# Optimization experiments

Hardware: AMD Instinct MI355X
Metric: run time of the kernel (lower is better)

The kernel has to match this reference:

```python
import jax, jax.numpy as jnp
import numpy as np

B, N, KNN_K = 4, 4096, 32
C1, C = 128, 256
K_SLOTS, RECON_M, N_RECON = 4, 96, 128
SLOT_ITERS = 3

def _ln(x, g, b):
    m = x.mean(-1, keepdims=True)
    v = jnp.var(x, axis=-1, keepdims=True)
    return (x - m) * jax.lax.rsqrt(v + 1e-5) * g + b

def _gather(f, idx):
    # f [B,P,C], idx [B,N,K] -> [B,N,K,C]
    return jax.vmap(lambda a, i: a[i])(f, idx)

def _knn(xyz, k):
    sq = jnp.sum(xyz * xyz, -1)
    d = sq[:, :, None] + sq[:, None, :] - 2.0 * jnp.einsum('bnc,bmc->bnm', xyz, xyz)
    return jax.lax.top_k(-d, k)[1]

def _conv_block(xyz, feats, W, b):
    # InterZPConv-style: KNN neighbor gather -> per-neighbor transform -> max aggregate
    idx = _knn(xyz, KNN_K)
    rel = _gather(xyz, idx) - xyz[:, :, None, :]
    h = jnp.concatenate([_gather(feats, idx), rel], axis=-1)
    h = jax.nn.relu(jnp.einsum('bnkc,cd->bnkd', h, W) + b)
    return h.max(axis=2)

def _bn(x, g, b):
    # BatchNorm2d (training mode) over (batch, slot) axes for 1x1-conv stacks
    m = x.mean(axis=(0, 1), keepdims=True)
    v = jnp.var(x, axis=(0, 1), keepdims=True)
    return (x - m) * jax.lax.rsqrt(v + 1e-5) * g + b

def _gru(upd, prev, W_ih, W_hh, b_ih, b_hh):
    gi = upd @ W_ih + b_ih
    gh = prev @ W_hh + b_hh
    r = jax.nn.sigmoid(gi[..., :C] + gh[..., :C])
    z = jax.nn.sigmoid(gi[..., C:2 * C] + gh[..., C:2 * C])
    n = jnp.tanh(gi[..., 2 * C:] + r * gh[..., 2 * C:])
    return (1.0 - z) * n + z * prev

def _chamfer(a, b):
    # a [B,M,3], b [B,P,3] -> (min over b per a-point, min over a per b-point), squared dists
    d = jnp.sum((a[..., :, None, :] - b[..., None, :, :]) ** 2, axis=-1)
    return d.min(axis=-1), d.min(axis=-2)

def _fps(pts):
    # farthest point sampling of N_RECON points from pts [P,3]
    P = pts.shape[0]
    d0 = jnp.full((P,), 1e10, pts.dtype)
    def step(carry, _):
        d, last = carry
        d = jnp.minimum(d, jnp.sum((pts - pts[last]) ** 2, axis=-1))
        nxt = jnp.argmax(d).astype(jnp.int32)
        return (d, nxt), nxt
    _, idxs = jax.lax.scan(step, (d0, jnp.array(0, jnp.int32)), None, length=N_RECON - 1)
    return jnp.concatenate([jnp.zeros((1,), jnp.int32), idxs])

def setup_inputs() -> dict:
    key = jax.random.key(0)
    ks = jax.random.split(key, 16)
    w = lambda k, s: jax.random.normal(k, s, jnp.float32) * 0.02
    z = lambda *s: jnp.zeros(s, jnp.float32)
    o = lambda *s: jnp.ones(s, jnp.float32)
    return {
        'x': jax.random.normal(ks[0], (B, 3, N), jnp.float32),
        'pose': jnp.zeros((B, N, 4, 4), jnp.float32),
        'W1': w(ks[1], (1 + 3, C1)), 'b1': z(C1),
        'W2': w(ks[2], (C1 + 3, C)), 'b2': z(C),
        'slots_mu': w(ks[3], (1, 1, C)), 'slots_sigma': jnp.abs(w(ks[4], (1, 1, C))) + 0.01,
        'ln_in_g': o(C), 'ln_in_b': z(C),
        'ln_slot_g': o(C), 'ln_slot_b': z(C),
        'ln_ff_g': o(C), 'ln_ff_b': z(C),
        'Wq': w(ks[5], (C, C)), 'Wk': w(ks[6], (C, C)), 'Wv': w(ks[7], (C, C)),
        'W_ih': w(ks[8], (C, 3 * C)), 'W_hh': w(ks[9], (C, 3 * C)),
        'b_ih': z(3 * C), 'b_hh': z(3 * C),
        'Wm1': w(ks[10], (C, C)), 'bm1': z(C),
        'Wm2': w(ks[11], (C, C)), 'bm2': z(C),
        'Wr1': w(ks[12], (C, C)), 'br1': z(C), 'g1': o(C), 'be1': z(C),
        'Wr2': w(ks[13], (C, C)), 'br2': z(C), 'g2': o(C), 'be2': z(C),
        'Wr3': w(ks[14], (C, RECON_M * 3)), 'br3': z(RECON_M * 3),
    }

def reference(x, pose, W1, b1, W2, b2, slots_mu, slots_sigma, ln_in_g, ln_in_b,
              ln_slot_g, ln_slot_b, ln_ff_g, ln_ff_b, Wq, Wk, Wv,
              W_ih, W_hh, b_ih, b_hh, Wm1, bm1, Wm2, bm2,
              Wr1, br1, g1, be1, Wr2, br2, g2, be2, Wr3, br3):
    xyz = jnp.transpose(x, (0, 2, 1))  # [B,N,3]
    feats = jnp.ones((B, N, 1), x.dtype)  # preprocess_input: unit features, na=1
    f = _conv_block(xyz, feats, W1, b1)   # [B,N,C1]
    f = _conv_block(xyz, f, W2, b2)       # [B,N,C]
    # Slot attention over per-point invariant features
    inp = _ln(f, ln_in_g, ln_in_b)
    kk = inp @ Wk
    vv = inp @ Wv
    slots = slots_mu + slots_sigma * jax.random.normal(jax.random.key(42), (B, K_SLOTS, C), x.dtype)
    scale = C ** -0.5
    attn = None
    for _ in range(SLOT_ITERS):
        prev = slots
        q = _ln(slots, ln_slot_g, ln_slot_b) @ Wq
        logits = scale * jnp.einsum('bkc,bnc->bkn', q, kk)
        attn = jax.nn.softmax(logits, axis=1)  # softmax over slots
        wgt = attn / (attn.sum(axis=-1, keepdims=True) + 1e-8)
        upd = jnp.einsum('bkn,bnc->bkc', wgt, vv)
        slots = _gru(upd, prev, W_ih, W_hh, b_ih, b_hh)
        h = _ln(slots, ln_ff_g, ln_ff_b)
        slots = slots + (jax.nn.relu(h @ Wm1 + bm1) @ Wm2 + bm2)
    attn_out = jnp.transpose(attn, (0, 2, 1))  # [B,N,K] (attn_ori.transpose(1,2))
    # Part reconstruction net (1x1 conv + BN + ReLU stack on slot features)
    h = jax.nn.relu(_bn(slots @ Wr1 + br1, g1, be1))
    h = jax.nn.relu(_bn(h @ Wr2 + br2, g2, be2))
    slot_points = (h @ Wr3 + br3).reshape(B, K_SLOTS, RECON_M, 3)
    all_pts = slot_points.reshape(B, K_SLOTS * RECON_M, 3)
    # FPS downsample + global chamfer against input points
    idx = jax.vmap(_fps)(all_pts)  # [B, N_RECON]
    ds = jnp.take_along_axis(all_pts, idx[..., None], axis=1)  # [B,N_RECON,3]
    d1, d2 = _chamfer(ds, xyz)
    loss = (d1.mean(-1) + d2.mean(-1)).mean()
    return loss, attn_out
```

## Files before the change

### kernel.cpp

```cpp
#include <hip/hip_runtime.h>

#define NBATCH 4
#define NPTS   4096
#define KNNK   32
#define C1D    128
#define CD     256
#define KPAD   160
#define ASTR   168
#define ASTR2  264

typedef _Float16 v8h __attribute__((ext_vector_type(8)));
typedef float    v4f __attribute__((ext_vector_type(4)));
typedef unsigned long long ull;


__device__ __forceinline__ float block_sum256(float v, float* red) {
    #pragma unroll
    for (int o = 32; o; o >>= 1) v += __shfl_down(v, o);
    __syncthreads();
    if ((threadIdx.x & 63) == 0) red[threadIdx.x >> 6] = v;
    __syncthreads();
    return red[0] + red[1] + red[2] + red[3];
}

__device__ __forceinline__ unsigned rotl32(unsigned x, unsigned r) {
    return (x << r) | (x >> (32u - r));
}

__device__ float erfinv_f(float x) {
    float w = -log1pf(-x * x);
    float p;
    if (w < 5.0f) {
        w -= 2.5f;
        p = 2.81022636e-08f;
        p = fmaf(p, w, 3.43273939e-07f);
        p = fmaf(p, w, -3.5233877e-06f);
        p = fmaf(p, w, -4.39150654e-06f);
        p = fmaf(p, w, 0.00021858087f);
        p = fmaf(p, w, -0.00125372503f);
        p = fmaf(p, w, -0.00417768164f);
        p = fmaf(p, w, 0.246640727f);
        p = fmaf(p, w, 1.50140941f);
    } else {
        w = sqrtf(w) - 3.0f;
        p = -0.000200214257f;
        p = fmaf(p, w, 0.000100950558f);
        p = fmaf(p, w, 0.00134934322f);
        p = fmaf(p, w, -0.00367342844f);
        p = fmaf(p, w, 0.00573950773f);
        p = fmaf(p, w, -0.0076224613f);
        p = fmaf(p, w, 0.00943887047f);
        p = fmaf(p, w, 1.00167406f);
        p = fmaf(p, w, 2.83297682f);
    }
    return p * x;
}

__device__ __forceinline__ float bits_to_normal(unsigned bits) {
    unsigned fb = (bits >> 9) | 0x3f800000u;
    float f = __uint_as_float(fb) - 1.0f;
    const float lo = -0.99999994f;
    float u = fmaf(f, 2.0f, lo);
    u = fmaxf(u, lo);
    return 1.41421356237f * erfinv_f(u);
}

__device__ __forceinline__ unsigned fmap(float f) {
    unsigned b = __float_as_uint(f);
    return (b & 0x80000000u) ? ~b : (b | 0x80000000u);
}

template <int CTRL, int RM>
__device__ __forceinline__ ull dpp_min_u64(ull k) {
    unsigned lo = (unsigned)k, hi = (unsigned)(k >> 32);
    unsigned tlo = (unsigned)__builtin_amdgcn_update_dpp((int)lo, (int)lo, CTRL, RM, 0xf, false);
    unsigned thi = (unsigned)__builtin_amdgcn_update_dpp((int)hi, (int)hi, CTRL, RM, 0xf, false);
    ull t = ((ull)thi << 32) | tlo;
    return t < k ? t : k;
}

template <int CTRL, int RM>
__device__ __forceinline__ void dpp_lexmax(float& v, int& ix) {
    int tv = __builtin_amdgcn_update_dpp(__float_as_int(v), __float_as_int(v), CTRL, RM, 0xf, false);
    int ti = __builtin_amdgcn_update_dpp(ix, ix, CTRL, RM, 0xf, false);
    float fv = __int_as_float(tv);
    bool take = (fv > v) || (fv == v && ti < ix);
    v  = take ? fv : v;
    ix = take ? ti : ix;
}


__global__ void prep_kernel(const float* __restrict__ x, float* __restrict__ xyz,
                            float4* __restrict__ xyzw) {
    int gid = blockIdx.x * 256 + threadIdx.x;
    if (gid >= NBATCH * NPTS) return;
    int b = gid >> 12, n = gid & (NPTS - 1);
    float a0 = x[(b * 3 + 0) * NPTS + n];
    float a1 = x[(b * 3 + 1) * NPTS + n];
    float a2 = x[(b * 3 + 2) * NPTS + n];
    xyz[gid * 3 + 0] = a0; xyz[gid * 3 + 1] = a1; xyz[gid * 3 + 2] = a2;
    float sq = a0 * a0 + a1 * a1 + a2 * a2;
    xyzw[gid] = make_float4(a0, a1, a2, sq);
}

__global__ void slots_init_kernel(const float* __restrict__ mu, const float* __restrict__ sg,
                                  float* __restrict__ slots, float* __restrict__ asum) {
    int j = blockIdx.x * 256 + threadIdx.x;
    if (j < 16) asum[j] = 0.0f;
    if (j >= 2048) return;
    unsigned ks0 = 0u, ks1 = 42u, ks2 = 0u ^ 42u ^ 0x1BD11BDAu;
    unsigned x0 = (unsigned)j + ks0;
    unsigned x1 = (unsigned)(j + 2048) + ks1;
    #define RND(r) { x0 += x1; x1 = rotl32(x1, r); x1 ^= x0; }
    RND(13u) RND(15u) RND(26u) RND(6u);  x0 += ks1; x1 += ks2 + 1u;
    RND(17u) RND(29u) RND(16u) RND(24u); x0 += ks2; x1 += ks0 + 2u;
    RND(13u) RND(15u) RND(26u) RND(6u);  x0 += ks0; x1 += ks1 + 3u;
    RND(17u) RND(29u) RND(16u) RND(24u); x0 += ks1; x1 += ks2 + 4u;
    RND(13u) RND(15u) RND(26u) RND(6u);  x0 += ks2; x1 += ks0 + 5u;
    #undef RND
    int c0 = j & 255, c1 = (j + 2048) & 255;
    slots[j]        = mu[c0] + sg[c0] * bits_to_normal(x0);
    slots[j + 2048] = mu[c1] + sg[c1] * bits_to_normal(x1);
}

__global__ __launch_bounds__(256) void knn_kernel(const float4* __restrict__ xyzw,
                                                  int* __restrict__ knn_idx) {
    int wid = threadIdx.x >> 6, lane = threadIdx.x & 63;
    int pid = blockIdx.x * 4 + wid;
    int b = pid >> 12, n = pid & (NPTS - 1);
    const float4* xb = xyzw + (size_t)b * NPTS;
    float4 p = xb[n];
    unsigned d[64];
    #pragma unroll
    for (int i = 0; i < 64; ++i) {
        float4 c = xb[i * 64 + lane];
        float dot = p.x * c.x + p.y * c.y + p.z * c.z;
        d[i] = fmap(p.w + c.w - 2.0f * dot);
    }
    unsigned gv[8]; int gi[8];
    #pragma unroll
    for (int g = 0; g < 8; ++g) {
        unsigned mv = d[g * 8]; int mi = g * 8;
        #pragma unroll
        for (int j = 1; j < 8; ++j)
            if (d[g * 8 + j] < mv) { mv = d[g * 8 + j]; mi = g * 8 + j; }
        gv[g] = mv; gi[g] = mi * 64 + lane;
    }
    unsigned lv = gv[0]; int li = gi[0];
    #pragma unroll
    for (int g = 1; g < 8; ++g)
        if (gv[g] < lv) { lv = gv[g]; li = gi[g]; }

    int* out = knn_idx + (size_t)pid * KNNK;
    #pragma unroll 1
    for (int s = 0; s < KNNK; ++s) {
        ull k = ((ull)lv << 32) | (unsigned)li;
        k = dpp_min_u64<0x111, 0xf>(k);
        k = dpp_min_u64<0x112, 0xf>(k);
        k = dpp_min_u64<0x114, 0xf>(k);
        k = dpp_min_u64<0x118, 0xf>(k);
        k = dpp_min_u64<0x142, 0xa>(k);
        k = dpp_min_u64<0x143, 0xc>(k);
        int fm = __builtin_amdgcn_readlane((int)(unsigned)k, 63);
        if (lane == 0) out[s] = fm;
        int flane = fm & 63;
        int slot  = fm >> 6;
        if (lane == flane) {
            int g = slot >> 3;
            #pragma unroll
            for (int g2 = 0; g2 < 8; ++g2) {
                if (g2 == g) {
                    #pragma unroll
                    for (int j = 0; j < 8; ++j)
                        if (g2 * 8 + j == slot) d[g2 * 8 + j] = 0xFFFFFFFFu;
                    unsigned mv = d[g2 * 8]; int mi = g2 * 8;
                    #pragma unroll
                    for (int j = 1; j < 8; ++j)
                        if (d[g2 * 8 + j] < mv) { mv = d[g2 * 8 + j]; mi = g2 * 8 + j; }
                    gv[g2] = mv; gi[g2] = mi * 64 + lane;
                }
            }
            lv = gv[0]; li = gi[0];
            #pragma unroll
            for (int g2 = 1; g2 < 8; ++g2)
                if (gv[g2] < lv) { lv = gv[g2]; li = gi[g2]; }
        }
    }
}

__global__ __launch_bounds__(128) void conv1_kernel(const float* __restrict__ xyz,
                                                    const int* __restrict__ knn_idx,
                                                    const float* __restrict__ W1,
                                                    const float* __restrict__ b1,
                                                    _Float16* __restrict__ f1h) {
    int pid = blockIdx.x;
    int b = pid >> 12, n = pid & (NPTS - 1);
    int d = threadIdx.x, lane = threadIdx.x & 63;
    const float* xb = xyz + (size_t)b * NPTS * 3;
    float w0 = W1[d], wx = W1[C1D + d], wy = W1[2 * C1D + d], wz = W1[3 * C1D + d];
    float bb = b1[d];
    float px = xb[n * 3], py = xb[n * 3 + 1], pz = xb[n * 3 + 2];
    const int* idx = knn_idx + (size_t)pid * KNNK;
    float cx = 0.0f, cy = 0.0f, cz = 0.0f;
    if (lane < 32) {
        int j = idx[lane];
        cx = xb[j * 3]; cy = xb[j * 3 + 1]; cz = xb[j * 3 + 2];
    }
    float m = -1e30f;
    #pragma unroll
    for (int k = 0; k < KNNK; ++k) {
        float jx = __shfl(cx, k), jy = __shfl(cy, k), jz = __shfl(cz, k);
        float v = w0 + bb + (jx - px) * wx + (jy - py) * wy + (jz - pz) * wz;
        m = fmaxf(m, v);
    }
    f1h[(size_t)pid * C1D + d] = (_Float16)fmaxf(m, 0.0f);
}

__global__ void w2t_kernel(const float* __restrict__ W2, _Float16* __restrict__ W2t) {
    int n = blockIdx.x;
    int k = threadIdx.x;
    W2t[n * KPAD + k] = (k < 131) ? (_Float16)W2[k * CD + n] : (_Float16)0.0f;
}

__global__ void wkvt_kernel(const float* __restrict__ Wk, const float* __restrict__ Wv,
                            _Float16* __restrict__ WkvT) {
    int n = blockIdx.x;
    int c = threadIdx.x;
    float v = (n < 256) ? Wk[c * CD + n] : Wv[c * CD + (n - 256)];
    WkvT[n * CD + c] = (_Float16)v;
}

__global__ __launch_bounds__(256) void conv2_mfma_kernel(const float* __restrict__ xyz,
                                                         const _Float16* __restrict__ f1h,
                                                         const int* __restrict__ knn_idx,
                                                         const _Float16* __restrict__ W2t,
                                                         const float* __restrict__ b2,
                                                         const float* __restrict__ g_in,
                                                         const float* __restrict__ b_in,
                                                         _Float16* __restrict__ inph) {
    __shared__ _Float16 A[64 * ASTR];
    __shared__ float colmax[2 * CD];
    __shared__ float red[4];
    int pid2 = blockIdx.x;
    int gp0 = pid2 * 2;
    int b = gp0 >> 12, n0 = gp0 & (NPTS - 1);
    int tid = threadIdx.x;
    const int* idx = knn_idx + (size_t)pid2 * 64;
    const float* xb = xyz + (size_t)b * NPTS * 3;

    {
        int r = tid & 63, seg = tid >> 6;
        int j = idx[r];
        const uint4* s4 = (const uint4*)(f1h + ((size_t)b * NPTS + j) * C1D);
        uint4* d4 = (uint4*)&A[r * ASTR];
        #pragma unroll
        for (int i = 0; i < 4; ++i) d4[seg * 4 + i] = s4[seg * 4 + i];
        unsigned* z = (unsigned*)&A[r * ASTR + 128];
        for (int i = seg; i < 20; i += 4) z[i] = 0u;
        int np_ = (r < 32) ? n0 : (n0 + 1);
        if (seg == 0) {
            A[r * ASTR + 128] = (_Float16)(xb[j * 3 + 0] - xb[np_ * 3 + 0]);
            A[r * ASTR + 129] = (_Float16)(xb[j * 3 + 1] - xb[np_ * 3 + 1]);
        } else if (seg == 1) {
            A[r * ASTR + 130] = (_Float16)(xb[j * 3 + 2] - xb[np_ * 3 + 2]);
        }
    }
    __syncthreads();

    int w = tid >> 6, lane = tid & 63, quad = lane >> 4, lr = lane & 15;
    v4f acc[4][4];
    #pragma unroll
    for (int rt = 0; rt < 4; ++rt)
        #pragma unroll
        for (int ct = 0; ct < 4; ++ct)
            acc[rt][ct] = (v4f){0.0f, 0.0f, 0.0f, 0.0f};

    #pragma unroll
    for (int kk = 0; kk < KPAD; kk += 32) {
        v8h af[4], bf[4];
        #pragma unroll
        for (int rt = 0; rt < 4; ++rt)
            af[rt] = *(const v8h*)&A[(rt * 16 + lr) * ASTR + kk + quad * 8];
        #pragma unroll
        for (int ct = 0; ct < 4; ++ct) {
            int ncol = w * 64 + ct * 16 + lr;
            bf[ct] = *(const v8h*)(W2t + (size_t)ncol * KPAD + kk + quad * 8);
        }
        #pragma unroll
        for (int rt = 0; rt < 4; ++rt)
            #pragma unroll
            for (int ct = 0; ct < 4; ++ct)
                acc[rt][ct] = __builtin_amdgcn_mfma_f32_16x16x32_f16(af[rt], bf[ct], acc[rt][ct], 0, 0, 0);
    }

    #pragma unroll
    for (int ct = 0; ct < 4; ++ct) {
        float tm[4];
        #pragma unroll
        for (int rt = 0; rt < 4; ++rt) {
            v4f a = acc[rt][ct];
            float v = fmaxf(fmaxf(a[0], a[1]), fmaxf(a[2], a[3]));
            v = fmaxf(v, __shfl_xor(v, 16));
            v = fmaxf(v, __shfl_xor(v, 32));
            tm[rt] = v;
        }
        float p0 = fmaxf(tm[0], tm[1]);
        float p1 = fmaxf(tm[2], tm[3]);
        if (quad == 0) {
            colmax[0 * CD + w * 64 + ct * 16 + lr] = p0;
            colmax[1 * CD + w * 64 + ct * 16 + lr] = p1;
        }
    }
    __syncthreads();

    int d = tid;
    #pragma unroll
    for (int p = 0; p < 2; ++p) {
        float v = fmaxf(colmax[p * CD + d] + b2[d], 0.0f);
        float s = block_sum256(v, red);
        float mean = s * (1.0f / 256.0f);
        float s2 = block_sum256(v * v, red);
        float var = s2 * (1.0f / 256.0f) - mean * mean;
        float iv = (v - mean) * rsqrtf(var + 1e-5f) * g_in[d] + b_in[d];
        inph[(size_t)(gp0 + p) * CD + d] = (_Float16)iv;
    }
}

__global__ __launch_bounds__(256) void kv_mfma_kernel(const _Float16* __restrict__ inph,
                                                      const _Float16* __restrict__ WkvT,
                                                      float* __restrict__ kk,
                                                      float* __restrict__ vv) {
    __shared__ _Float16 A[64 * ASTR2];
    int rb = blockIdx.x >> 1, half = blockIdx.x & 1;
    int row0 = rb * 64;
    int tid = threadIdx.x;
    {
        const uint4* src4 = (const uint4*)(inph + (size_t)row0 * CD);
        #pragma unroll
        for (int i = 0; i < 8; ++i) {
            int idx = i * 256 + tid;
            int row = idx >> 5, c8 = idx & 31;
            *(uint4*)&A[row * ASTR2 + c8 * 8] = src4[idx];
        }
    }
    __syncthreads();
    int w = tid >> 6, lane = tid & 63, quad = lane >> 4, lr = lane & 15;
    v4f acc[4][4];
    #pragma unroll
    for (int rt = 0; rt < 4; ++rt)
        #pragma unroll
        for (int ct = 0; ct < 4; ++ct)
            acc[rt][ct] = (v4f){0.0f, 0.0f, 0.0f, 0.0f};
    #pragma unroll
    for (int ks = 0; ks < CD; ks += 32) {
        v8h af[4], bf[4];
        #pragma unroll
        for (int rt = 0; rt < 4; ++rt)
            af[rt] = *(const v8h*)&A[(rt * 16 + lr) * ASTR2 + ks + quad * 8];
        #pragma unroll
        for (int ct = 0; ct < 4; ++ct) {
            int ncol = half * 256 + w * 64 + ct * 16 + lr;
            bf[ct] = *(const v8h*)(WkvT + (size_t)ncol * CD + ks + quad * 8);
        }
        #pragma unroll
        for (int rt = 0; rt < 4; ++rt)
            #pragma unroll
            for (int ct = 0; ct < 4; ++ct)
                acc[rt][ct] = __builtin_amdgcn_mfma_f32_16x16x32_f16(af[rt], bf[ct], acc[rt][ct], 0, 0, 0);
    }
    float* dst = half ? vv : kk;
    #pragma unroll
    for (int rt = 0; rt < 4; ++rt)
        #pragma unroll
        for (int ct = 0; ct < 4; ++ct) {
            int col = w * 64 + ct * 16 + lr;
            #pragma unroll
            for (int r = 0; r < 4; ++r) {
                int row = rt * 16 + quad * 4 + r;
                dst[(size_t)(row0 + row) * CD + col] = acc[rt][ct][r];
            }
        }
}

__global__ __launch_bounds__(256) void slotq_kernel(const float* __restrict__ slots,
                                                    const float* __restrict__ g_sl,
                                                    const float* __restrict__ b_sl,
                                                    const float* __restrict__ Wq,
                                                    float* __restrict__ q) {
    int row = blockIdx.x;
    int d = threadIdx.x;
    __shared__ float sl[CD];
    __shared__ float red[4];
    float v = slots[row * CD + d];
    float s = block_sum256(v, red);
    float mean = s * (1.0f / 256.0f);
    float s2 = block_sum256(v * v, red);
    float var = s2 * (1.0f / 256.0f) - mean * mean;
    float ln = (v - mean) * rsqrtf(var + 1e-5f) * g_sl[d] + b_sl[d];
    sl[d] = ln;
    __syncthreads();
    float acc = 0.0f;
    const float4* sp = (const float4*)sl;
    for (int c4 = 0; c4 < 64; ++c4) {
        float4 x = sp[c4];
        int cb = c4 * 4;
        acc += x.x * Wq[cb * CD + d] + x.y * Wq[(cb + 1) * CD + d]
             + x.z * Wq[(cb + 2) * CD + d] + x.w * Wq[(cb + 3) * CD + d];
    }
    q[row * CD + d] = acc;
}

__global__ __launch_bounds__(256) void attn_updp_kernel(const float* __restrict__ q,
                                                        const float* __restrict__ kk,
                                                        const float* __restrict__ vv,
                                                        float* __restrict__ asum,
                                                        float* __restrict__ updp,
                                                        float* __restrict__ out_attn) {
    int b = blockIdx.x >> 4;
    int chunk = blockIdx.x & 15;
    int t = threadIdx.x;
    __shared__ float qs[4 * CD];
    __shared__ float aw[256 * 4];
    __shared__ float redk[16];
    for (int i = t; i < 4 * CD; i += 256) qs[i] = q[b * 4 * CD + i];
    __syncthreads();

    int n = chunk * 256 + t;
    const float4* kp = (const float4*)(kk + ((size_t)b * NPTS + n) * CD);
    const float4* q0 = (const float4*)(qs);
    const float4* q1 = (const float4*)(qs + CD);
    const float4* q2 = (const float4*)(qs + 2 * CD);
    const float4* q3 = (const float4*)(qs + 3 * CD);
    float a0 = 0, a1 = 0, a2 = 0, a3 = 0;
    for (int c4 = 0; c4 < 64; ++c4) {
        float4 kv = kp[c4];
        float4 x;
        x = q0[c4]; a0 += kv.x * x.x + kv.y * x.y + kv.z * x.z + kv.w * x.w;
        x = q1[c4]; a1 += kv.x * x.x + kv.y * x.y + kv.z * x.z + kv.w * x.w;
        x = q2[c4]; a2 += kv.x * x.x + kv.y * x.y + kv.z * x.z + kv.w * x.w;
        x = q3[c4]; a3 += kv.x * x.x + kv.y * x.y + kv.z * x.z + kv.w * x.w;
    }
    const float scale = 0.0625f;
    float l0 = scale * a0, l1 = scale * a1, l2 = scale * a2, l3 = scale * a3;
    float mx = fmaxf(fmaxf(l0, l1), fmaxf(l2, l3));
    float e0 = expf(l0 - mx), e1 = expf(l1 - mx), e2 = expf(l2 - mx), e3 = expf(l3 - mx);
    float inv = 1.0f / (e0 + e1 + e2 + e3);
    e0 *= inv; e1 *= inv; e2 *= inv; e3 *= inv;
    aw[t * 4 + 0] = e0; aw[t * 4 + 1] = e1; aw[t * 4 + 2] = e2; aw[t * 4 + 3] = e3;
    if (out_attn) {
        float* o = out_attn + ((size_t)b * NPTS + n) * 4;
        o[0] = e0; o[1] = e1; o[2] = e2; o[3] = e3;
    }
    float as[4] = {e0, e1, e2, e3};
    #pragma unroll
    for (int k = 0; k < 4; ++k) {
        float v = as[k];
        #pragma unroll
        for (int o = 32; o; o >>= 1) v += __shfl_down(v, o);
        if ((t & 63) == 0) redk[(t >> 6) * 4 + k] = v;
    }
    __syncthreads();
    if (t < 4) {
        float s = redk[t] + redk[4 + t] + redk[8 + t] + redk[12 + t];
        atomicAdd(&asum[b * 4 + t], s);
    }

    float ac0 = 0.0f, ac1 = 0.0f, ac2 = 0.0f, ac3 = 0.0f;
    const float* vb = vv + ((size_t)b * NPTS + chunk * 256) * CD;
    for (int nn2 = 0; nn2 < 256; ++nn2) {
        float v = vb[(size_t)nn2 * CD + t];
        float4 w4 = *(const float4*)&aw[nn2 * 4];
        ac0 += w4.x * v; ac1 += w4.y * v; ac2 += w4.z * v; ac3 += w4.w * v;
    }
    updp[((size_t)(b * 4 + 0) * 16 + chunk) * CD + t] = ac0;
    updp[((size_t)(b * 4 + 1) * 16 + chunk) * CD + t] = ac1;
    updp[((size_t)(b * 4 + 2) * 16 + chunk) * CD + t] = ac2;
    updp[((size_t)(b * 4 + 3) * 16 + chunk) * CD + t] = ac3;
}

__global__ __launch_bounds__(256) void gru_gates_kernel(const float* __restrict__ updp,
                                                        const float* __restrict__ asum,
                                                        const float* __restrict__ slots,
                                                        const float* __restrict__ W_ih,
                                                        const float* __restrict__ W_hh,
                                                        const float* __restrict__ b_ih,
                                                        const float* __restrict__ b_hh,
                                                        float* __restrict__ gi,
                                                        float* __restrict__ gh) {
    int row = blockIdx.x / 3, gate = blockIdx.x % 3;
    int d = threadIdx.x;
    __shared__ float su[CD], sp[CD];
    float f = 1.0f / (asum[row] + 1e-8f);
    float u = 0.0f;
    for (int p = 0; p < 16; ++p) u += updp[((size_t)row * 16 + p) * CD + d];
    u *= f;
    su[d] = u; sp[d] = slots[row * CD + d];
    __syncthreads();
    float acc_i = b_ih[gate * CD + d];
    float acc_h = b_hh[gate * CD + d];
    const float* wi = W_ih + gate * CD + d;
    const float* wh = W_hh + gate * CD + d;
    for (int c = 0; c < CD; ++c) {
        acc_i += su[c] * wi[c * 3 * CD];
        acc_h += sp[c] * wh[c * 3 * CD];
    }
    gi[row * 3 * CD + gate * CD + d] = acc_i;
    gh[row * 3 * CD + gate * CD + d] = acc_h;
}

__global__ __launch_bounds__(256) void gru_mlp_kernel(const float* __restrict__ gi,
                                                      const float* __restrict__ gh,
                                                      float* __restrict__ slots,
                                                      const float* __restrict__ g_ff,
                                                      const float* __restrict__ b_ff,
                                                      const float* __restrict__ Wm1,
                                                      const float* __restrict__ bm1,
                                                      const float* __restrict__ Wm2,
                                                      const float* __restrict__ bm2,
                                                      float* __restrict__ asum) {
    int row = blockIdx.x;
    int d = threadIdx.x;
    __shared__ float sh[CD];
    __shared__ float red[4];
    float prev = slots[row * CD + d];
    float gir = gi[row * 3 * CD + d], giz = gi[row * 3 * CD + CD + d], gin = gi[row * 3 * CD + 2 * CD + d];
    float ghr = gh[row * 3 * CD + d], ghz = gh[row * 3 * CD + CD + d], ghn = gh[row * 3 * CD + 2 * CD + d];
    if (d == 0) asum[row] = 0.0f;
    float r = 1.0f / (1.0f + expf(-(gir + ghr)));
    float z = 1.0f / (1.0f + expf(-(giz + ghz)));
    float nn = tanhf(gin + r * ghn);
    float sNew = (1.0f - z) * nn + z * prev;
    float s = block_sum256(sNew, red);
    float mean = s * (1.0f / 256.0f);
    float s2 = block_sum256(sNew * sNew, red);
    float var = s2 * (1.0f / 256.0f) - mean * mean;
    float h = (sNew - mean) * rsqrtf(var + 1e-5f) * g_ff[d] + b_ff[d];
    __syncthreads();
    sh[d] = h;
    __syncthreads();
    float y = bm1[d];
    {
        const float4* hp = (const float4*)sh;
        for (int c4 = 0; c4 < 64; ++c4) {
            float4 x = hp[c4];
            int cb = c4 * 4;
            y += x.x * Wm1[cb * CD + d] + x.y * Wm1[(cb + 1) * CD + d]
               + x.z * Wm1[(cb + 2) * CD + d] + x.w * Wm1[(cb + 3) * CD + d];
        }
    }
    y = fmaxf(y, 0.0f);
    __syncthreads();
    sh[d] = y;
    __syncthreads();
    float o = bm2[d];
    {
        const float4* hp = (const float4*)sh;
        for (int c4 = 0; c4 < 64; ++c4) {
            float4 x = hp[c4];
            int cb = c4 * 4;
            o += x.x * Wm2[cb * CD + d] + x.y * Wm2[(cb + 1) * CD + d]
               + x.z * Wm2[(cb + 2) * CD + d] + x.w * Wm2[(cb + 3) * CD + d];
        }
    }
    slots[row * CD + d] = sNew + o;
}

__global__ __launch_bounds__(320) void recon_kernel(const float* __restrict__ slots,
                                                    const float* __restrict__ Wr1, const float* __restrict__ br1,
                                                    const float* __restrict__ g1, const float* __restrict__ be1,
                                                    const float* __restrict__ Wr2, const float* __restrict__ br2,
                                                    const float* __restrict__ g2, const float* __restrict__ be2,
                                                    const float* __restrict__ Wr3, const float* __restrict__ br3,
                                                    float* __restrict__ spts) {
    __shared__ float sl[16 * CD];
    __shared__ float h1[16 * CD];
    __shared__ float h2[16 * CD];
    int d = threadIdx.x;
    if (d < CD) for (int r = 0; r < 16; ++r) sl[r * CD + d] = slots[r * CD + d];
    __syncthreads();
    if (d < CD) {
        float t[16];
        #pragma unroll
        for (int r = 0; r < 16; ++r) t[r] = br1[d];
        for (int c4 = 0; c4 < 64; ++c4) {
            int cb = c4 * 4;
            float w0 = Wr1[cb * CD + d], w1 = Wr1[(cb + 1) * CD + d];
            float w2 = Wr1[(cb + 2) * CD + d], w3 = Wr1[(cb + 3) * CD + d];
            #pragma unroll
            for (int r = 0; r < 16; ++r) {
                float4 x = *(const float4*)(sl + r * CD + cb);
                t[r] += x.x * w0 + x.y * w1 + x.z * w2 + x.w * w3;
            }
        }
        float mean = 0.0f;
        for (int r = 0; r < 16; ++r) mean += t[r];
        mean *= (1.0f / 16.0f);
        float var = 0.0f;
        for (int r = 0; r < 16; ++r) { float dd = t[r] - mean; var += dd * dd; }
        var *= (1.0f / 16.0f);
        float inv = rsqrtf(var + 1e-5f);
        for (int r = 0; r < 16; ++r)
            h1[r * CD + d] = fmaxf(0.0f, (t[r] - mean) * inv * g1[d] + be1[d]);
    }
    __syncthreads();
    if (d < CD) {
        float t[16];
        #pragma unroll
        for (int r = 0; r < 16; ++r) t[r] = br2[d];
        for (int c4 = 0; c4 < 64; ++c4) {
            int cb = c4 * 4;
            float w0 = Wr2[cb * CD + d], w1 = Wr2[(cb + 1) * CD + d];
            float w2 = Wr2[(cb + 2) * CD + d], w3 = Wr2[(cb + 3) * CD + d];
            #pragma unroll
            for (int r = 0; r < 16; ++r) {
                float4 x = *(const float4*)(h1 + r * CD + cb);
                t[r] += x.x * w0 + x.y * w1 + x.z * w2 + x.w * w3;
            }
        }
        float mean = 0.0f;
        for (int r = 0; r < 16; ++r) mean += t[r];
        mean *= (1.0f / 16.0f);
        float var = 0.0f;
        for (int r = 0; r < 16; ++r) { float dd = t[r] - mean; var += dd * dd; }
        var *= (1.0f / 16.0f);
        float inv = rsqrtf(var + 1e-5f);
        for (int r = 0; r < 16; ++r)
            h2[r * CD + d] = fmaxf(0.0f, (t[r] - mean) * inv * g2[d] + be2[d]);
    }
    __syncthreads();
    if (d < 288) {
        float t[16];
        #pragma unroll
        for (int r = 0; r < 16; ++r) t[r] = br3[d];
        for (int c4 = 0; c4 < 64; ++c4) {
            int cb = c4 * 4;
            float w0 = Wr3[cb * 288 + d], w1 = Wr3[(cb + 1) * 288 + d];
            float w2 = Wr3[(cb + 2) * 288 + d], w3 = Wr3[(cb + 3) * 288 + d];
            #pragma unroll
            for (int r = 0; r < 16; ++r) {
                float4 x = *(const float4*)(h2 + r * CD + cb);
                t[r] += x.x * w0 + x.y * w1 + x.z * w2 + x.w * w3;
            }
        }
        for (int r = 0; r < 16; ++r) spts[r * 288 + d] = t[r];
    }
}

__global__ __launch_bounds__(64) void fps_kernel(const float* __restrict__ spts,
                                                 int* __restrict__ fidx,
                                                 float* __restrict__ lacc,
                                                 unsigned* __restrict__ mnbuf) {
    int b = blockIdx.x;
    int lane = threadIdx.x;
    const float* pts = spts + (size_t)b * 384 * 3;
    int* out = fidx + b * 128;
    if (lane == 0) out[0] = 0;
    if (b == 0 && lane == 0) lacc[0] = 0.0f;
    mnbuf[b * 128 + lane] = 0x7F800000u;
    mnbuf[b * 128 + 64 + lane] = 0x7F800000u;
    float px[6], py[6], pz[6], dd[6];
    #pragma unroll
    for (int i = 0; i < 6; ++i) {
        int m = i * 64 + lane;
        px[i] = pts[m * 3]; py[i] = pts[m * 3 + 1]; pz[i] = pts[m * 3 + 2];
        dd[i] = 1e10f;
    }
    float lx = pts[0], ly = pts[1], lz = pts[2];
    #pragma unroll 1
    for (int s = 1; s < 128; ++s) {
        #pragma unroll
        for (int i = 0; i < 6; ++i) {
            float dx = px[i] - lx, dy = py[i] - ly, dz = pz[i] - lz;
            dd[i] = fminf(dd[i], dx * dx + dy * dy + dz * dz);
        }
        float bv = dd[0]; int bi = lane;
        #pragma unroll
        for (int i = 1; i < 6; ++i)
            if (dd[i] > bv) { bv = dd[i]; bi = i * 64 + lane; }
        dpp_lexmax<0x111, 0xf>(bv, bi);
        dpp_lexmax<0x112, 0xf>(bv, bi);
        dpp_lexmax<0x114, 0xf>(bv, bi);
        dpp_lexmax<0x118, 0xf>(bv, bi);
        dpp_lexmax<0x142, 0xa>(bv, bi);
        dpp_lexmax<0x143, 0xc>(bv, bi);
        int fm = __builtin_amdgcn_readlane(bi, 63);
        if (lane == 0) out[s] = fm;
        int slot = fm >> 6, sl_lane = fm & 63;
        float sx = px[0], sy = py[0], sz = pz[0];
        #pragma unroll
        for (int i = 1; i < 6; ++i)
            if (slot == i) { sx = px[i]; sy = py[i]; sz = pz[i]; }
        lx = __int_as_float(__builtin_amdgcn_readlane(__float_as_int(sx), sl_lane));
        ly = __int_as_float(__builtin_amdgcn_readlane(__float_as_int(sy), sl_lane));
        lz = __int_as_float(__builtin_amdgcn_readlane(__float_as_int(sz), sl_lane));
    }
}

__global__ __launch_bounds__(256) void chamfer_sum2_kernel(const float* __restrict__ spts,
                                                           const int* __restrict__ fidx,
                                                           const float* __restrict__ xyz,
                                                           float* __restrict__ lacc) {
    int b = blockIdx.x >> 4, chunk = blockIdx.x & 15;
    int t = threadIdx.x;
    __shared__ float ds[128 * 3];
    __shared__ float red[4];
    const float* pts = spts + (size_t)b * 384 * 3;
    if (t < 128) {
        int j = fidx[b * 128 + t];
        ds[t * 3] = pts[j * 3]; ds[t * 3 + 1] = pts[j * 3 + 1]; ds[t * 3 + 2] = pts[j * 3 + 2];
    }
    __syncthreads();
    int n = chunk * 256 + t;
    const float* xb = xyz + (size_t)b * NPTS * 3;
    float px = xb[n * 3], py = xb[n * 3 + 1], pz = xb[n * 3 + 2];
    float mn = 1e30f;
    #pragma unroll 4
    for (int jj = 0; jj < 128; ++jj) {
        float dx = ds[jj * 3] - px, dy = ds[jj * 3 + 1] - py, dz = ds[jj * 3 + 2] - pz;
        mn = fminf(mn, dx * dx + dy * dy + dz * dz);
    }
    float total = block_sum256(mn * (1.0f / 4096.0f), red);
    if (t == 0) atomicAdd(lacc, total);
}

__global__ __launch_bounds__(128) void chamfer_min1_kernel(const float* __restrict__ spts,
                                                           const int* __restrict__ fidx,
                                                           const float* __restrict__ xyz,
                                                           unsigned* __restrict__ mnbuf) {
    int b = blockIdx.x >> 4, chunk = blockIdx.x & 15;
    int t = threadIdx.x;
    __shared__ float tile[256 * 3];
    const float* xb = xyz + ((size_t)b * NPTS + chunk * 256) * 3;
    for (int i = t; i < 768; i += 128) tile[i] = xb[i];
    __syncthreads();
    int j = fidx[b * 128 + t];
    const float* pts = spts + (size_t)b * 384 * 3;
    float px = pts[j * 3], py = pts[j * 3 + 1], pz = pts[j * 3 + 2];
    float mn = 1e30f;
    #pragma unroll 4
    for (int i = 0; i < 256; ++i) {
        float dx = tile[i * 3] - px, dy = tile[i * 3 + 1] - py, dz = tile[i * 3 + 2] - pz;
        mn = fminf(mn, dx * dx + dy * dy + dz * dz);
    }
    atomicMin(&mnbuf[b * 128 + t], __float_as_uint(mn));
}

__global__ __launch_bounds__(512) void chamfer_final_kernel(const unsigned* __restrict__ mnbuf,
                                                            const float* __restrict__ lacc,
                                                            float* __restrict__ out) {
    int t = threadIdx.x;
    __shared__ float r[8];
    float v = __uint_as_float(mnbuf[t]) * (1.0f / 128.0f);
    #pragma unroll
    for (int o = 32; o; o >>= 1) v += __shfl_down(v, o);
    if ((t & 63) == 0) r[t >> 6] = v;
    __syncthreads();
    if (t == 0) {
        float tot = 0.0f;
        #pragma unroll
        for (int i = 0; i < 8; ++i) tot += r[i];
        out[0] = (lacc[0] + tot) * 0.25f;
    }
}


extern "C" void kernel_launch(void* const* d_in, const int* in_sizes, int n_in,
                              void* d_out, int out_size, void* d_ws, size_t ws_size,
                              hipStream_t stream) {
    (void)in_sizes; (void)n_in; (void)out_size; (void)ws_size;
    const float* x    = (const float*)d_in[0];
    const float* W1   = (const float*)d_in[2];
    const float* b1   = (const float*)d_in[3];
    const float* W2   = (const float*)d_in[4];
    const float* b2   = (const float*)d_in[5];
    const float* mu   = (const float*)d_in[6];
    const float* sg   = (const float*)d_in[7];
    const float* g_in = (const float*)d_in[8];
    const float* b_in = (const float*)d_in[9];
    const float* g_sl = (const float*)d_in[10];
    const float* b_sl = (const float*)d_in[11];
    const float* g_ff = (const float*)d_in[12];
    const float* b_ff = (const float*)d_in[13];
    const float* Wq   = (const float*)d_in[14];
    const float* Wk   = (const float*)d_in[15];
    const float* Wv   = (const float*)d_in[16];
    const float* W_ih = (const float*)d_in[17];
    const float* W_hh = (const float*)d_in[18];
    const float* b_ih = (const float*)d_in[19];
    const float* b_hh = (const float*)d_in[20];
    const float* Wm1  = (const float*)d_in[21];
    const float* bm1  = (const float*)d_in[22];
    const float* Wm2  = (const float*)d_in[23];
    const float* bm2  = (const float*)d_in[24];
    const float* Wr1  = (const float*)d_in[25];
    const float* br1  = (const float*)d_in[26];
    const float* g1   = (const float*)d_in[27];
    const float* be1  = (const float*)d_in[28];
    const float* Wr2  = (const float*)d_in[29];
    const float* br2  = (const float*)d_in[30];
    const float* g2   = (const float*)d_in[31];
    const float* be2  = (const float*)d_in[32];
    const float* Wr3  = (const float*)d_in[33];
    const float* br3  = (const float*)d_in[34];

    float* ws    = (float*)d_ws;
    float* xyz   = ws;
    float* xyzw  = xyz + 49152;
    int*   knn   = (int*)(xyzw + 65536);
    _Float16* f1h = (_Float16*)(knn + 524288);
    _Float16* W2t = (_Float16*)((float*)f1h + 1048576);
    _Float16* WkvT = (_Float16*)((float*)W2t + 20480);
    _Float16* inph = (_Float16*)((float*)WkvT + 65536);
    float* kkb   = (float*)inph + 2097152;
    float* vvb   = kkb + 4194304;
    float* slots = vvb + 4194304;
    float* qb    = slots + 4096;
    float* asum  = qb + 4096;
    float* updp  = asum + 16;
    float* gi    = updp + 65536;
    float* gh    = gi + 12288;
    float* spts  = gh + 12288;
    int*   fidx  = (int*)(spts + 4608);
    float* lacc  = (float*)(fidx + 512);
    unsigned* mnbuf = (unsigned*)(lacc + 1);

    float* out = (float*)d_out;

    prep_kernel<<<64, 256, 0, stream>>>(x, xyz, (float4*)xyzw);
    slots_init_kernel<<<8, 256, 0, stream>>>(mu, sg, slots, asum);
    knn_kernel<<<NBATCH * NPTS / 4, 256, 0, stream>>>((const float4*)xyzw, knn);
    conv1_kernel<<<NBATCH * NPTS, 128, 0, stream>>>(xyz, knn, W1, b1, f1h);
    w2t_kernel<<<256, 160, 0, stream>>>(W2, W2t);
    wkvt_kernel<<<512, 256, 0, stream>>>(Wk, Wv, WkvT);
    conv2_mfma_kernel<<<NBATCH * NPTS / 2, 256, 0, stream>>>(xyz, f1h, knn, W2t, b2, g_in, b_in, inph);
    kv_mfma_kernel<<<NBATCH * NPTS / 64 * 2, 256, 0, stream>>>(inph, WkvT, kkb, vvb);

    for (int it = 0; it < 3; ++it) {
        slotq_kernel<<<16, 256, 0, stream>>>(slots, g_sl, b_sl, Wq, qb);
        attn_updp_kernel<<<64, 256, 0, stream>>>(qb, kkb, vvb, asum, updp,
                                                 (it == 2) ? (out + 1) : (float*)nullptr);
        gru_gates_kernel<<<48, 256, 0, stream>>>(updp, asum, slots, W_ih, W_hh, b_ih, b_hh, gi, gh);
        gru_mlp_kernel<<<16, 256, 0, stream>>>(gi, gh, slots, g_ff, b_ff, Wm1, bm1, Wm2, bm2, asum);
    }

    recon_kernel<<<1, 320, 0, stream>>>(slots, Wr1, br1, g1, be1, Wr2, br2, g2, be2, Wr3, br3, spts);
    fps_kernel<<<4, 64, 0, stream>>>(spts, fidx, lacc, mnbuf);
    chamfer_sum2_kernel<<<64, 256, 0, stream>>>(spts, fidx, xyz, lacc);
    chamfer_min1_kernel<<<64, 128, 0, stream>>>(spts, fidx, xyz, mnbuf);
    chamfer_final_kernel<<<1, 512, 0, stream>>>(mnbuf, lacc, out);
}
```

Measured before the change: 741.6 us.

## Merge small kernels and spread slot-attention and GRU gate work over more blocks

Folds slot initialisation into prep_kernel, merges the two weight-transpose kernels into one, and merges the two chamfer kernels into one launch, removing several launches. The attention kernel now uses 256 blocks with one wave per slot and 64 points per block instead of 64 blocks, and the GRU gate kernel splits its reduction into halves over 96 blocks. Both are meant to raise parallelism in the latency-bound slot iterations. In exchange, the partial-sum buffers grow and the GRU gate kernel has to sum 64 partials instead of 16.

```diff
diff --git a/kernel.cpp b/kernel.cpp
--- a/kernel.cpp
+++ b/kernel.cpp
@@ -91,7 +91,9 @@
 
 
 __global__ void prep_kernel(const float* __restrict__ x, float* __restrict__ xyz,
-                            float4* __restrict__ xyzw) {
+                            float4* __restrict__ xyzw,
+                            const float* __restrict__ mu, const float* __restrict__ sg,
+                            float* __restrict__ slots, float* __restrict__ asum) {
     int gid = blockIdx.x * 256 + threadIdx.x;
     if (gid >= NBATCH * NPTS) return;
     int b = gid >> 12, n = gid & (NPTS - 1);
@@ -101,26 +103,23 @@
     xyz[gid * 3 + 0] = a0; xyz[gid * 3 + 1] = a1; xyz[gid * 3 + 2] = a2;
     float sq = a0 * a0 + a1 * a1 + a2 * a2;
     xyzw[gid] = make_float4(a0, a1, a2, sq);
-}
-
-__global__ void slots_init_kernel(const float* __restrict__ mu, const float* __restrict__ sg,
-                                  float* __restrict__ slots, float* __restrict__ asum) {
-    int j = blockIdx.x * 256 + threadIdx.x;
-    if (j < 16) asum[j] = 0.0f;
-    if (j >= 2048) return;
-    unsigned ks0 = 0u, ks1 = 42u, ks2 = 0u ^ 42u ^ 0x1BD11BDAu;
-    unsigned x0 = (unsigned)j + ks0;
-    unsigned x1 = (unsigned)(j + 2048) + ks1;
-    #define RND(r) { x0 += x1; x1 = rotl32(x1, r); x1 ^= x0; }
-    RND(13u) RND(15u) RND(26u) RND(6u);  x0 += ks1; x1 += ks2 + 1u;
-    RND(17u) RND(29u) RND(16u) RND(24u); x0 += ks2; x1 += ks0 + 2u;
-    RND(13u) RND(15u) RND(26u) RND(6u);  x0 += ks0; x1 += ks1 + 3u;
-    RND(17u) RND(29u) RND(16u) RND(24u); x0 += ks1; x1 += ks2 + 4u;
-    RND(13u) RND(15u) RND(26u) RND(6u);  x0 += ks2; x1 += ks0 + 5u;
-    #undef RND
-    int c0 = j & 255, c1 = (j + 2048) & 255;
-    slots[j]        = mu[c0] + sg[c0] * bits_to_normal(x0);
-    slots[j + 2048] = mu[c1] + sg[c1] * bits_to_normal(x1);
+    if (gid < 16) asum[gid] = 0.0f;
+    if (gid < 2048) {
+        int j = gid;
+        unsigned ks0 = 0u, ks1 = 42u, ks2 = 0u ^ 42u ^ 0x1BD11BDAu;
+        unsigned x0 = (unsigned)j + ks0;
+        unsigned x1 = (unsigned)(j + 2048) + ks1;
+        #define RND(r) { x0 += x1; x1 = rotl32(x1, r); x1 ^= x0; }
+        RND(13u) RND(15u) RND(26u) RND(6u);  x0 += ks1; x1 += ks2 + 1u;
+        RND(17u) RND(29u) RND(16u) RND(24u); x0 += ks2; x1 += ks0 + 2u;
+        RND(13u) RND(15u) RND(26u) RND(6u);  x0 += ks0; x1 += ks1 + 3u;
+        RND(17u) RND(29u) RND(16u) RND(24u); x0 += ks1; x1 += ks2 + 4u;
+        RND(13u) RND(15u) RND(26u) RND(6u);  x0 += ks2; x1 += ks0 + 5u;
+        #undef RND
+        int c0 = j & 255, c1 = (j + 2048) & 255;
+        slots[j]        = mu[c0] + sg[c0] * bits_to_normal(x0);
+        slots[j + 2048] = mu[c1] + sg[c1] * bits_to_normal(x1);
+    }
 }
 
 __global__ __launch_bounds__(256) void knn_kernel(const float4* __restrict__ xyzw,
@@ -216,18 +215,19 @@
     f1h[(size_t)pid * C1D + d] = (_Float16)fmaxf(m, 0.0f);
 }
 
-__global__ void w2t_kernel(const float* __restrict__ W2, _Float16* __restrict__ W2t) {
-    int n = blockIdx.x;
-    int k = threadIdx.x;
-    W2t[n * KPAD + k] = (k < 131) ? (_Float16)W2[k * CD + n] : (_Float16)0.0f;
-}
-
-__global__ void wkvt_kernel(const float* __restrict__ Wk, const float* __restrict__ Wv,
-                            _Float16* __restrict__ WkvT) {
-    int n = blockIdx.x;
-    int c = threadIdx.x;
-    float v = (n < 256) ? Wk[c * CD + n] : Wv[c * CD + (n - 256)];
-    WkvT[n * CD + c] = (_Float16)v;
+__global__ __launch_bounds__(256) void wtrans_kernel(const float* __restrict__ W2,
+                                                     const float* __restrict__ Wk,
+                                                     const float* __restrict__ Wv,
+                                                     _Float16* __restrict__ W2t,
+                                                     _Float16* __restrict__ WkvT) {
+    int nb = blockIdx.x, t = threadIdx.x;
+    if (nb < 256) {
+        if (t < KPAD) W2t[nb * KPAD + t] = (t < 131) ? (_Float16)W2[t * CD + nb] : (_Float16)0.0f;
+    } else {
+        int n = nb - 256;
+        float v = (n < 256) ? Wk[t * CD + n] : Wv[t * CD + (n - 256)];
+        WkvT[n * CD + t] = (_Float16)v;
+    }
 }
 
 __global__ __launch_bounds__(256) void conv2_mfma_kernel(const float* __restrict__ xyz,
@@ -416,66 +416,67 @@
                                                         float* __restrict__ asum,
                                                         float* __restrict__ updp,
                                                         float* __restrict__ out_attn) {
-    int b = blockIdx.x >> 4;
-    int chunk = blockIdx.x & 15;
+    int b = blockIdx.x >> 6;
+    int chunk = blockIdx.x & 63;
     int t = threadIdx.x;
     __shared__ float qs[4 * CD];
-    __shared__ float aw[256 * 4];
-    __shared__ float redk[16];
+    __shared__ float logit[64 * 4];
+    __shared__ float aw[64 * 4];
     for (int i = t; i < 4 * CD; i += 256) qs[i] = q[b * 4 * CD + i];
     __syncthreads();
 
-    int n = chunk * 256 + t;
-    const float4* kp = (const float4*)(kk + ((size_t)b * NPTS + n) * CD);
-    const float4* q0 = (const float4*)(qs);
-    const float4* q1 = (const float4*)(qs + CD);
-    const float4* q2 = (const float4*)(qs + 2 * CD);
-    const float4* q3 = (const float4*)(qs + 3 * CD);
-    float a0 = 0, a1 = 0, a2 = 0, a3 = 0;
-    for (int c4 = 0; c4 < 64; ++c4) {
-        float4 kv = kp[c4];
-        float4 x;
-        x = q0[c4]; a0 += kv.x * x.x + kv.y * x.y + kv.z * x.z + kv.w * x.w;
-        x = q1[c4]; a1 += kv.x * x.x + kv.y * x.y + kv.z * x.z + kv.w * x.w;
-        x = q2[c4]; a2 += kv.x * x.x + kv.y * x.y + kv.z * x.z + kv.w * x.w;
-        x = q3[c4]; a3 += kv.x * x.x + kv.y * x.y + kv.z * x.z + kv.w * x.w;
-    }
-    const float scale = 0.0625f;
-    float l0 = scale * a0, l1 = scale * a1, l2 = scale * a2, l3 = scale * a3;
-    float mx = fmaxf(fmaxf(l0, l1), fmaxf(l2, l3));
-    float e0 = expf(l0 - mx), e1 = expf(l1 - mx), e2 = expf(l2 - mx), e3 = expf(l3 - mx);
-    float inv = 1.0f / (e0 + e1 + e2 + e3);
-    e0 *= inv; e1 *= inv; e2 *= inv; e3 *= inv;
-    aw[t * 4 + 0] = e0; aw[t * 4 + 1] = e1; aw[t * 4 + 2] = e2; aw[t * 4 + 3] = e3;
-    if (out_attn) {
-        float* o = out_attn + ((size_t)b * NPTS + n) * 4;
-        o[0] = e0; o[1] = e1; o[2] = e2; o[3] = e3;
-    }
-    float as[4] = {e0, e1, e2, e3};
-    #pragma unroll
-    for (int k = 0; k < 4; ++k) {
-        float v = as[k];
-        #pragma unroll
-        for (int o = 32; o; o >>= 1) v += __shfl_down(v, o);
-        if ((t & 63) == 0) redk[(t >> 6) * 4 + k] = v;
-    }
-    __syncthreads();
-    if (t < 4) {
-        float s = redk[t] + redk[4 + t] + redk[8 + t] + redk[12 + t];
-        atomicAdd(&asum[b * 4 + t], s);
-    }
+    int p = t & 63, r = t >> 6;
+    int n = chunk * 64 + p;
+    {
+        const float4* kp = (const float4*)(kk + ((size_t)b * NPTS + n) * CD);
+        const float4* qr = (const float4*)(qs + r * CD);
+        float a = 0.0f;
+        for (int c4 = 0; c4 < 64; ++c4) {
+            float4 kv = kp[c4];
+            float4 x = qr[c4];
+            a += kv.x * x.x + kv.y * x.y + kv.z * x.z + kv.w * x.w;
+        }
+        logit[p * 4 + r] = 0.0625f * a;
+    }
+    __syncthreads();
+    if (t < 64) {
+        float l0 = logit[t * 4 + 0], l1 = logit[t * 4 + 1];
+        float l2 = logit[t * 4 + 2], l3 = logit[t * 4 + 3];
+        float mx = fmaxf(fmaxf(l0, l1), fmaxf(l2, l3));
+        float e0 = expf(l0 - mx), e1 = expf(l1 - mx), e2 = expf(l2 - mx), e3 = expf(l3 - mx);
+        float inv = 1.0f / (e0 + e1 + e2 + e3);
+        e0 *= inv; e1 *= inv; e2 *= inv; e3 *= inv;
+        aw[t * 4 + 0] = e0; aw[t * 4 + 1] = e1; aw[t * 4 + 2] = e2; aw[t * 4 + 3] = e3;
+        if (out_attn) {
+            float* o = out_attn + ((size_t)b * NPTS + chunk * 64 + t) * 4;
+            o[0] = e0; o[1] = e1; o[2] = e2; o[3] = e3;
+        }
+        float s0 = e0, s1 = e1, s2 = e2, s3 = e3;
+        #pragma unroll
+        for (int o = 32; o; o >>= 1) {
+            s0 += __shfl_down(s0, o); s1 += __shfl_down(s1, o);
+            s2 += __shfl_down(s2, o); s3 += __shfl_down(s3, o);
+        }
+        if (t == 0) {
+            atomicAdd(&asum[b * 4 + 0], s0);
+            atomicAdd(&asum[b * 4 + 1], s1);
+            atomicAdd(&asum[b * 4 + 2], s2);
+            atomicAdd(&asum[b * 4 + 3], s3);
+        }
+    }
+    __syncthreads();
 
     float ac0 = 0.0f, ac1 = 0.0f, ac2 = 0.0f, ac3 = 0.0f;
-    const float* vb = vv + ((size_t)b * NPTS + chunk * 256) * CD;
-    for (int nn2 = 0; nn2 < 256; ++nn2) {
+    const float* vb = vv + ((size_t)b * NPTS + chunk * 64) * CD;
+    for (int nn2 = 0; nn2 < 64; ++nn2) {
         float v = vb[(size_t)nn2 * CD + t];
         float4 w4 = *(const float4*)&aw[nn2 * 4];
         ac0 += w4.x * v; ac1 += w4.y * v; ac2 += w4.z * v; ac3 += w4.w * v;
     }
-    updp[((size_t)(b * 4 + 0) * 16 + chunk) * CD + t] = ac0;
-    updp[((size_t)(b * 4 + 1) * 16 + chunk) * CD + t] = ac1;
-    updp[((size_t)(b * 4 + 2) * 16 + chunk) * CD + t] = ac2;
-    updp[((size_t)(b * 4 + 3) * 16 + chunk) * CD + t] = ac3;
+    updp[((size_t)(b * 4 + 0) * 64 + chunk) * CD + t] = ac0;
+    updp[((size_t)(b * 4 + 1) * 64 + chunk) * CD + t] = ac1;
+    updp[((size_t)(b * 4 + 2) * 64 + chunk) * CD + t] = ac2;
+    updp[((size_t)(b * 4 + 3) * 64 + chunk) * CD + t] = ac3;
 }
 
 __global__ __launch_bounds__(256) void gru_gates_kernel(const float* __restrict__ updp,
@@ -487,25 +488,28 @@
                                                         const float* __restrict__ b_hh,
                                                         float* __restrict__ gi,
                                                         float* __restrict__ gh) {
-    int row = blockIdx.x / 3, gate = blockIdx.x % 3;
+    int idx = blockIdx.x;
+    int row = idx / 6, rem = idx % 6;
+    int gate = rem >> 1, half = rem & 1;
     int d = threadIdx.x;
     __shared__ float su[CD], sp[CD];
     float f = 1.0f / (asum[row] + 1e-8f);
     float u = 0.0f;
-    for (int p = 0; p < 16; ++p) u += updp[((size_t)row * 16 + p) * CD + d];
+    for (int p = 0; p < 64; ++p) u += updp[((size_t)row * 64 + p) * CD + d];
     u *= f;
     su[d] = u; sp[d] = slots[row * CD + d];
     __syncthreads();
-    float acc_i = b_ih[gate * CD + d];
-    float acc_h = b_hh[gate * CD + d];
+    float acc_i = half ? 0.0f : b_ih[gate * CD + d];
+    float acc_h = half ? 0.0f : b_hh[gate * CD + d];
     const float* wi = W_ih + gate * CD + d;
     const float* wh = W_hh + gate * CD + d;
-    for (int c = 0; c < CD; ++c) {
+    int c0 = half * 128;
+    for (int c = c0; c < c0 + 128; ++c) {
         acc_i += su[c] * wi[c * 3 * CD];
         acc_h += sp[c] * wh[c * 3 * CD];
     }
-    gi[row * 3 * CD + gate * CD + d] = acc_i;
-    gh[row * 3 * CD + gate * CD + d] = acc_h;
+    gi[((size_t)(row * 3 + gate) * 2 + half) * CD + d] = acc_i;
+    gh[((size_t)(row * 3 + gate) * 2 + half) * CD + d] = acc_h;
 }
 
 __global__ __launch_bounds__(256) void gru_mlp_kernel(const float* __restrict__ gi,
@@ -523,8 +527,12 @@
     __shared__ float sh[CD];
     __shared__ float red[4];
     float prev = slots[row * CD + d];
-    float gir = gi[row * 3 * CD + d], giz = gi[row * 3 * CD + CD + d], gin = gi[row * 3 * CD + 2 * CD + d];
-    float ghr = gh[row * 3 * CD + d], ghz = gh[row * 3 * CD + CD + d], ghn = gh[row * 3 * CD + 2 * CD + d];
+    float gir = gi[((size_t)(row * 3 + 0) * 2 + 0) * CD + d] + gi[((size_t)(row * 3 + 0) * 2 + 1) * CD + d];
+    float giz = gi[((size_t)(row * 3 + 1) * 2 + 0) * CD + d] + gi[((size_t)(row * 3 + 1) * 2 + 1) * CD + d];
+    float gin = gi[((size_t)(row * 3 + 2) * 2 + 0) * CD + d] + gi[((size_t)(row * 3 + 2) * 2 + 1) * CD + d];
+    float ghr = gh[((size_t)(row * 3 + 0) * 2 + 0) * CD + d] + gh[((size_t)(row * 3 + 0) * 2 + 1) * CD + d];
+    float ghz = gh[((size_t)(row * 3 + 1) * 2 + 0) * CD + d] + gh[((size_t)(row * 3 + 1) * 2 + 1) * CD + d];
+    float ghn = gh[((size_t)(row * 3 + 2) * 2 + 0) * CD + d] + gh[((size_t)(row * 3 + 2) * 2 + 1) * CD + d];
     if (d == 0) asum[row] = 0.0f;
     float r = 1.0f / (1.0f + expf(-(gir + ghr)));
     float z = 1.0f / (1.0f + expf(-(giz + ghz)));
@@ -696,53 +704,53 @@
     }
 }
 
-__global__ __launch_bounds__(256) void chamfer_sum2_kernel(const float* __restrict__ spts,
-                                                           const int* __restrict__ fidx,
-                                                           const float* __restrict__ xyz,
-                                                           float* __restrict__ lacc) {
-    int b = blockIdx.x >> 4, chunk = blockIdx.x & 15;
+__global__ __launch_bounds__(256) void chamfer_kernel(const float* __restrict__ spts,
+                                                      const int* __restrict__ fidx,
+                                                      const float* __restrict__ xyz,
+                                                      float* __restrict__ lacc,
+                                                      unsigned* __restrict__ mnbuf) {
     int t = threadIdx.x;
-    __shared__ float ds[128 * 3];
-    __shared__ float red[4];
-    const float* pts = spts + (size_t)b * 384 * 3;
-    if (t < 128) {
-        int j = fidx[b * 128 + t];
-        ds[t * 3] = pts[j * 3]; ds[t * 3 + 1] = pts[j * 3 + 1]; ds[t * 3 + 2] = pts[j * 3 + 2];
-    }
-    __syncthreads();
-    int n = chunk * 256 + t;
-    const float* xb = xyz + (size_t)b * NPTS * 3;
-    float px = xb[n * 3], py = xb[n * 3 + 1], pz = xb[n * 3 + 2];
-    float mn = 1e30f;
-    #pragma unroll 4
-    for (int jj = 0; jj < 128; ++jj) {
-        float dx = ds[jj * 3] - px, dy = ds[jj * 3 + 1] - py, dz = ds[jj * 3 + 2] - pz;
-        mn = fminf(mn, dx * dx + dy * dy + dz * dz);
-    }
-    float total = block_sum256(mn * (1.0f / 4096.0f), red);
-    if (t == 0) atomicAdd(lacc, total);
-}
-
-__global__ __launch_bounds__(128) void chamfer_min1_kernel(const float* __restrict__ spts,
-                                                           const int* __restrict__ fidx,
-                                                           const float* __restrict__ xyz,
-                                                           unsigned* __restrict__ mnbuf) {
-    int b = blockIdx.x >> 4, chunk = blockIdx.x & 15;
-    int t = threadIdx.x;
-    __shared__ float tile[256 * 3];
-    const float* xb = xyz + ((size_t)b * NPTS + chunk * 256) * 3;
-    for (int i = t; i < 768; i += 128) tile[i] = xb[i];
-    __syncthreads();
-    int j = fidx[b * 128 + t];
-    const float* pts = spts + (size_t)b * 384 * 3;
-    float px = pts[j * 3], py = pts[j * 3 + 1], pz = pts[j * 3 + 2];
-    float mn = 1e30f;
-    #pragma unroll 4
-    for (int i = 0; i < 256; ++i) {
-        float dx = tile[i * 3] - px, dy = tile[i * 3 + 1] - py, dz = tile[i * 3 + 2] - pz;
-        mn = fminf(mn, dx * dx + dy * dy + dz * dz);
-    }
-    atomicMin(&mnbuf[b * 128 + t], __float_as_uint(mn));
+    if (blockIdx.x < 64) {
+        int b = blockIdx.x >> 4, chunk = blockIdx.x & 15;
+        __shared__ float ds[128 * 3];
+        __shared__ float red[4];
+        const float* pts = spts + (size_t)b * 384 * 3;
+        if (t < 128) {
+            int j = fidx[b * 128 + t];
+            ds[t * 3] = pts[j * 3]; ds[t * 3 + 1] = pts[j * 3 + 1]; ds[t * 3 + 2] = pts[j * 3 + 2];
+        }
+        __syncthreads();
+        int n = chunk * 256 + t;
+        const float* xb = xyz + (size_t)b * NPTS * 3;
+        float px = xb[n * 3], py = xb[n * 3 + 1], pz = xb[n * 3 + 2];
+        float mn = 1e30f;
+        #pragma unroll 4
+        for (int jj = 0; jj < 128; ++jj) {
+            float dx = ds[jj * 3] - px, dy = ds[jj * 3 + 1] - py, dz = ds[jj * 3 + 2] - pz;
+            mn = fminf(mn, dx * dx + dy * dy + dz * dz);
+        }
+        float total = block_sum256(mn * (1.0f / 4096.0f), red);
+        if (t == 0) atomicAdd(lacc, total);
+    } else {
+        int bid = blockIdx.x - 64;
+        int b = bid >> 4, chunk = bid & 15;
+        __shared__ float tile[256 * 3];
+        const float* xb = xyz + ((size_t)b * NPTS + chunk * 256) * 3;
+        for (int i = t; i < 768; i += 256) tile[i] = xb[i];
+        __syncthreads();
+        if (t < 128) {
+            int j = fidx[b * 128 + t];
+            const float* pts = spts + (size_t)b * 384 * 3;
+            float px = pts[j * 3], py = pts[j * 3 + 1], pz = pts[j * 3 + 2];
+            float mn = 1e30f;
+            #pragma unroll 4
+            for (int i = 0; i < 256; ++i) {
+                float dx = tile[i * 3] - px, dy = tile[i * 3 + 1] - py, dz = tile[i * 3 + 2] - pz;
+                mn = fminf(mn, dx * dx + dy * dy + dz * dz);
+            }
+            atomicMin(&mnbuf[b * 128 + t], __float_as_uint(mn));
+        }
+    }
 }
 
 __global__ __launch_bounds__(512) void chamfer_final_kernel(const unsigned* __restrict__ mnbuf,
@@ -817,35 +825,32 @@
     float* qb    = slots + 4096;
     float* asum  = qb + 4096;
     float* updp  = asum + 16;
-    float* gi    = updp + 65536;
-    float* gh    = gi + 12288;
-    float* spts  = gh + 12288;
+    float* gi    = updp + 262144;
+    float* gh    = gi + 24576;
+    float* spts  = gh + 24576;
     int*   fidx  = (int*)(spts + 4608);
     float* lacc  = (float*)(fidx + 512);
     unsigned* mnbuf = (unsigned*)(lacc + 1);
 
     float* out = (float*)d_out;
 
-    prep_kernel<<<64, 256, 0, stream>>>(x, xyz, (float4*)xyzw);
-    slots_init_kernel<<<8, 256, 0, stream>>>(mu, sg, slots, asum);
+    prep_kernel<<<64, 256, 0, stream>>>(x, xyz, (float4*)xyzw, mu, sg, slots, asum);
     knn_kernel<<<NBATCH * NPTS / 4, 256, 0, stream>>>((const float4*)xyzw, knn);
     conv1_kernel<<<NBATCH * NPTS, 128, 0, stream>>>(xyz, knn, W1, b1, f1h);
-    w2t_kernel<<<256, 160, 0, stream>>>(W2, W2t);
-    wkvt_kernel<<<512, 256, 0, stream>>>(Wk, Wv, WkvT);
+    wtrans_kernel<<<768, 256, 0, stream>>>(W2, Wk, Wv, W2t, WkvT);
     conv2_mfma_kernel<<<NBATCH * NPTS / 2, 256, 0, stream>>>(xyz, f1h, knn, W2t, b2, g_in, b_in, inph);
     kv_mfma_kernel<<<NBATCH * NPTS / 64 * 2, 256, 0, stream>>>(inph, WkvT, kkb, vvb);
 
     for (int it = 0; it < 3; ++it) {
         slotq_kernel<<<16, 256, 0, stream>>>(slots, g_sl, b_sl, Wq, qb);
-        attn_updp_kernel<<<64, 256, 0, stream>>>(qb, kkb, vvb, asum, updp,
-                                                 (it == 2) ? (out + 1) : (float*)nullptr);
-        gru_gates_kernel<<<48, 256, 0, stream>>>(updp, asum, slots, W_ih, W_hh, b_ih, b_hh, gi, gh);
+        attn_updp_kernel<<<256, 256, 0, stream>>>(qb, kkb, vvb, asum, updp,
+                                                  (it == 2) ? (out + 1) : (float*)nullptr);
+        gru_gates_kernel<<<96, 256, 0, stream>>>(updp, asum, slots, W_ih, W_hh, b_ih, b_hh, gi, gh);
         gru_mlp_kernel<<<16, 256, 0, stream>>>(gi, gh, slots, g_ff, b_ff, Wm1, bm1, Wm2, bm2, asum);
     }
 
     recon_kernel<<<1, 320, 0, stream>>>(slots, Wr1, br1, g1, be1, Wr2, br2, g2, be2, Wr3, br3, spts);
     fps_kernel<<<4, 64, 0, stream>>>(spts, fidx, lacc, mnbuf);
-    chamfer_sum2_kernel<<<64, 256, 0, stream>>>(spts, fidx, xyz, lacc);
-    chamfer_min1_kernel<<<64, 128, 0, stream>>>(spts, fidx, xyz, mnbuf);
+    chamfer_kernel<<<128, 256, 0, stream>>>(spts, fidx, xyz, lacc, mnbuf);
     chamfer_final_kernel<<<1, 512, 0, stream>>>(mnbuf, lacc, out);
 }
```

After: 715.0 us. -3.6%, faster.
